# Kernel tuning notes

Hardware: AMD Instinct MI355X
Metric: run time of the kernel (lower is better)

## Reference

```python
import jax, jax.numpy as jnp
import numpy as np

N, E, G = 100000, 400000, 4096
H, C = 4, 32            # heads, hidden_dim per head
D_OUT = H * C           # 128
NODE_D, EDGE_D = 38, 13
DEC_H, OUT_D = 64, 1
NEG_SLOPE = 0.2
LN_EPS = 1e-5


def setup_inputs() -> dict:
    key = jax.random.key(0)
    ks = jax.random.split(key, 40)
    r = lambda k, s: jax.random.normal(k, s, jnp.float32) * 0.1
    inp = {
        "x": jax.random.normal(ks[0], (N, NODE_D), jnp.float32),
        "edge_index": jax.random.randint(ks[1], (2, E), 0, N),
        "edge_attr": jax.random.uniform(ks[2], (E, EDGE_D), jnp.float32),
        "batch": jnp.sort(jax.random.randint(ks[3], (N,), 0, G)),
        # --- block 1 (in=38) ---
        "Wl1": r(ks[4], (NODE_D, D_OUT)), "bl1": jnp.zeros((D_OUT,), jnp.float32),
        "Wr1": r(ks[5], (NODE_D, D_OUT)), "br1": jnp.zeros((D_OUT,), jnp.float32),
        "We1": r(ks[6], (EDGE_D, D_OUT)),
        "att1": r(ks[7], (H, C)), "ab1": jnp.zeros((D_OUT,), jnp.float32),
        "ln_g1": jnp.ones((D_OUT,), jnp.float32), "ln_b1": jnp.zeros((D_OUT,), jnp.float32),
        "Wres": r(ks[8], (NODE_D, D_OUT)), "bres": jnp.zeros((D_OUT,), jnp.float32),
        # --- block 2 (in=128, residual = identity) ---
        "Wl2": r(ks[9], (D_OUT, D_OUT)), "bl2": jnp.zeros((D_OUT,), jnp.float32),
        "Wr2": r(ks[10], (D_OUT, D_OUT)), "br2": jnp.zeros((D_OUT,), jnp.float32),
        "We2": r(ks[11], (EDGE_D, D_OUT)),
        "att2": r(ks[12], (H, C)), "ab2": jnp.zeros((D_OUT,), jnp.float32),
        "ln_g2": jnp.ones((D_OUT,), jnp.float32), "ln_b2": jnp.zeros((D_OUT,), jnp.float32),
        # --- readout MLP ---
        "Wd1": r(ks[13], (D_OUT, DEC_H)), "bd1": jnp.zeros((DEC_H,), jnp.float32),
        "Wd2": r(ks[14], (DEC_H, OUT_D)), "bd2": jnp.zeros((OUT_D,), jnp.float32),
    }
    return inp


def _segment_softmax(logits, seg, n):
    m = jax.ops.segment_max(logits, seg, num_segments=n)
    ex = jnp.exp(logits - m[seg])
    s = jax.ops.segment_sum(ex, seg, num_segments=n)
    return ex / s[seg]


def _gatv2(x, src, dst, e_feat, Wl, bl, Wr, br, We, att, ab):
    n = x.shape[0]
    xl = (x @ Wl + bl).reshape(n, H, C)   # source transform
    xr = (x @ Wr + br).reshape(n, H, C)   # target transform
    ee = (e_feat @ We).reshape(-1, H, C)  # edge transform
    z = jax.nn.leaky_relu(xl[src] + xr[dst] + ee, NEG_SLOPE)  # [E,H,C]
    logits = jnp.einsum('ehc,hc->eh', z, att)                 # [E,H]
    alpha = _segment_softmax(logits, dst, n)                  # softmax over target nbhd
    out = jax.ops.segment_sum(xl[src] * alpha[..., None], dst, num_segments=n)
    return out.reshape(n, D_OUT) + ab


def _layernorm(h, g, b):
    mu = jnp.mean(h, -1, keepdims=True)
    d = h - mu
    v = jnp.mean(d * d, -1, keepdims=True)
    return d * jax.lax.rsqrt(v + LN_EPS) * g + b


def reference(x, edge_index, edge_attr, batch,
              Wl1, bl1, Wr1, br1, We1, att1, ab1, ln_g1, ln_b1, Wres, bres,
              Wl2, bl2, Wr2, br2, We2, att2, ab2, ln_g2, ln_b2,
              Wd1, bd1, Wd2, bd2):
    src, dst = edge_index[0], edge_index[1]
    n = x.shape[0]
    # add_self_loops(fill_value='mean'): self-loop edge attr = mean of incoming edge attrs
    deg = jax.ops.segment_sum(jnp.ones((src.shape[0],), x.dtype), dst, num_segments=n)
    loop_attr = jax.ops.segment_sum(edge_attr, dst, num_segments=n) / jnp.clip(deg, 1.0)[:, None]
    nodes = jnp.arange(n)
    src_a = jnp.concatenate([src, nodes])
    dst_a = jnp.concatenate([dst, nodes])
    ea = jnp.concatenate([edge_attr, loop_attr], axis=0)

    # block 1
    h = _gatv2(x, src_a, dst_a, ea, Wl1, bl1, Wr1, br1, We1, att1, ab1)
    h = jax.nn.elu(h)
    h = _layernorm(h + (x @ Wres + bres), ln_g1, ln_b1)
    # block 2 (identity residual)
    h2 = _gatv2(h, src_a, dst_a, ea, Wl2, bl2, Wr2, br2, We2, att2, ab2)
    h2 = jax.nn.elu(h2)
    h2 = _layernorm(h2 + h, ln_g2, ln_b2)

    # global mean pool over graphs
    cnt = jax.ops.segment_sum(jnp.ones((n,), x.dtype), batch, num_segments=G)
    g = jax.ops.segment_sum(h2, batch, num_segments=G) / jnp.clip(cnt, 1.0)[:, None]

    return jax.nn.relu(g @ Wd1 + bd1) @ Wd2 + bd2
```

## Files before the change

kernel.cpp:

```cpp
#include <hip/hip_runtime.h>

typedef unsigned short u16;
typedef unsigned int   u32;
typedef __attribute__((ext_vector_type(8))) short short8;
typedef __attribute__((ext_vector_type(4))) float float4v;
typedef __attribute__((ext_vector_type(2))) float float2v;

#define NODE_D   38
#define EDGE_D   13
#define D_OUT    128
#define NEG_SLOPE 0.2f
#define LN_EPS   1e-5f

__device__ __forceinline__ float bf2f(u16 v) { return __uint_as_float(((u32)v) << 16); }
__device__ __forceinline__ u16 f2bf(float f) {
    u32 u = __float_as_uint(f);
    u += 0x7fffu + ((u >> 16) & 1u);
    return (u16)(u >> 16);
}

template <int CTRL>
__device__ __forceinline__ float dpp_radd(float x) {
    int t = __builtin_amdgcn_update_dpp(0, __float_as_int(x), CTRL, 0xf, 0xf, true);
    return x + __int_as_float(t);
}
__device__ __forceinline__ float reduce16(float p) {
    p = dpp_radd<0xB1>(p);
    p = dpp_radd<0x4E>(p);
    p = dpp_radd<0x124>(p);
    p = dpp_radd<0x128>(p);
    return p;
}
__device__ __forceinline__ float reduce64(float v) {
    v = reduce16(v);
    v += __shfl_xor(v, 16, 64);
    v += __shfl_xor(v, 32, 64);
    return v;
}

__global__ void k_pre(const int* __restrict__ dst, int E, int* __restrict__ deg,
                      const int* __restrict__ batch, int N, int G, int* __restrict__ goff,
                      const float* __restrict__ x, u16* __restrict__ xb) {
    int i = blockIdx.x * blockDim.x + threadIdx.x;
    if (i < E) atomicAdd(deg + dst[i], 1);
    if (i < N) {
        int b = batch[i];
        int prev = (i == 0) ? -1 : batch[i - 1];
        for (int g = prev + 1; g <= b; g++) goff[g] = i;
        if (i == N - 1)
            for (int g = b + 1; g <= G; g++) goff[g] = N;
    }
    if (i < N * 32) {
        int n = i >> 5, kk = (i & 31) * 2;
        float f0 = (kk < NODE_D) ? x[(size_t)n * NODE_D + kk] : 0.f;
        float f1 = (kk + 1 < NODE_D) ? x[(size_t)n * NODE_D + kk + 1] : 0.f;
        ((u32*)xb)[(size_t)n * 32 + (i & 31)] = (u32)f2bf(f0) | ((u32)f2bf(f1) << 16);
    }
}

#define SCAN_CHUNK 1024
__global__ void k_scan1(const int* __restrict__ cnt, int N, int addone, int* __restrict__ bsum) {
    __shared__ int sh[256];
    int base = blockIdx.x * SCAN_CHUNK;
    int t = threadIdx.x;
    int s = 0;
#pragma unroll
    for (int i = 0; i < 4; i++) { int idx = base + t * 4 + i; if (idx < N) s += cnt[idx] + addone; }
    sh[t] = s; __syncthreads();
    for (int ofs = 128; ofs > 0; ofs >>= 1) {
        if (t < ofs) sh[t] += sh[t + ofs];
        __syncthreads();
    }
    if (t == 0) bsum[blockIdx.x] = sh[0];
}
__global__ void k_scan2(const int* __restrict__ bsum, int nb, int* __restrict__ boff) {
    __shared__ int sh[256];
    int t = threadIdx.x;
    if (nb <= 256) {
        int v = (t < nb) ? bsum[t] : 0;
        sh[t] = v; __syncthreads();
        for (int ofs = 1; ofs < 256; ofs <<= 1) {
            int x = (t >= ofs) ? sh[t - ofs] : 0;
            __syncthreads();
            sh[t] += x;
            __syncthreads();
        }
        if (t < nb) boff[t] = sh[t] - v;
        if (t == nb - 1) boff[nb] = sh[t];
    } else if (t == 0) {
        int run = 0;
        for (int i = 0; i < nb; i++) { boff[i] = run; run += bsum[i]; }
        boff[nb] = run;
    }
}
__global__ void k_scan3(const int* __restrict__ cnt, int N, int addone,
                        const int* __restrict__ boff, int nb, int* __restrict__ off) {
    __shared__ int wtot[4];
    int base = blockIdx.x * SCAN_CHUNK;
    int t = threadIdx.x;
    int lane = t & 63, w = t >> 6;
    int v[4]; int s = 0;
#pragma unroll
    for (int i = 0; i < 4; i++) { int idx = base + t * 4 + i; v[i] = (idx < N) ? cnt[idx] + addone : 0; s += v[i]; }
    int inc = s;
#pragma unroll
    for (int ofs = 1; ofs < 64; ofs <<= 1) {
        int x = __shfl_up(inc, ofs, 64);
        if (lane >= ofs) inc += x;
    }
    if (lane == 63) wtot[w] = inc;
    __syncthreads();
    int wofs = 0;
    for (int i = 0; i < w; i++) wofs += wtot[i];
    int run = boff[blockIdx.x] + wofs + (inc - s);
#pragma unroll
    for (int i = 0; i < 4; i++) {
        int idx = base + t * 4 + i;
        if (idx < N) off[idx] = run;
        run += v[i];
    }
    if (blockIdx.x == 0 && t == 0) off[N] = boff[nb];
}

__global__ void k_fill(const int* __restrict__ src, const int* __restrict__ dst,
                       const float* __restrict__ eattr, int E,
                       const int* __restrict__ csr_off, int* __restrict__ fill,
                       int* __restrict__ csr_src, u16* __restrict__ A) {
    int e = blockIdx.x * blockDim.x + threadIdx.x;
    if (e >= E) return;
    int d = dst[e];
    int pos = csr_off[d] + atomicAdd(fill + d, 1);
    csr_src[pos] = src[e];
    u16 row[16];
#pragma unroll
    for (int k = 0; k < EDGE_D; k++) row[k] = f2bf(eattr[(size_t)e * EDGE_D + k]);
#pragma unroll
    for (int k = EDGE_D; k < 16; k++) row[k] = 0;
    uint4* rp = (uint4*)(A + (size_t)pos * 16);
    rp[0] = (uint4){(u32)row[0] | ((u32)row[1] << 16), (u32)row[2] | ((u32)row[3] << 16),
                    (u32)row[4] | ((u32)row[5] << 16), (u32)row[6] | ((u32)row[7] << 16)};
    rp[1] = (uint4){(u32)row[8] | ((u32)row[9] << 16), (u32)row[10] | ((u32)row[11] << 16),
                    (u32)row[12] | ((u32)row[13] << 16), (u32)row[14] | ((u32)row[15] << 16)};
}

__global__ void k_self(const int* __restrict__ csr_off, int N,
                       int* __restrict__ csr_src, u16* __restrict__ A) {
    int tid = blockIdx.x * blockDim.x + threadIdx.x;
    if (tid >= N * 16) return;
    int n = tid >> 4, k = tid & 15;
    int b = csr_off[n], e2 = csr_off[n + 1] - 1;
    u16 v = 0;
    if (k < EDGE_D) {
        float s = 0.f;
        for (int j = b; j < e2; j++) s += bf2f(A[(size_t)j * 16 + k]);
        v = f2bf(s / fmaxf((float)(e2 - b), 1.f));
    }
    A[(size_t)e2 * 16 + k] = v;
    if (k == 0) csr_src[e2] = n;
}

template <int KPAD, int CT, int KREAL, bool IN_BF16>
__global__ __launch_bounds__(256) void k_tf_mfma(
    const void* __restrict__ in_v,
    const float* __restrict__ W0, const float* __restrict__ b0,
    const float* __restrict__ W1, const float* __restrict__ b1,
    const float* __restrict__ W2, const float* __restrict__ b2,
    u16* __restrict__ o0, u16* __restrict__ o1, u16* __restrict__ o2,
    int N) {
    constexpr int RS = KPAD + 8;
    __shared__ u16 Bsw[CT * 16 * RS];
    __shared__ float bsh[CT * 16];
    const float* Ws[3] = {W0, W1, W2};
    const float* bs[3] = {b0, b1, b2};
    u16* outs[3] = {o0, o1, o2};
    int t = threadIdx.x;
    for (int i = t; i < CT * 16 * KPAD; i += 256) {
        int c = i / KPAD, k = i - c * KPAD;
        float v = (k < KREAL) ? Ws[c >> 7][(size_t)k * 128 + (c & 127)] : 0.f;
        Bsw[c * RS + k] = f2bf(v);
    }
    for (int i = t; i < CT * 16; i += 256) bsh[i] = bs[i >> 7][i & 127];
    __syncthreads();

    int wid = t >> 6, lane = t & 63;
    int quad = lane >> 4, m = lane & 15;

    for (int g0 = blockIdx.x * 64; g0 < N; g0 += gridDim.x * 64) {
        int na = g0 + wid * 16 + m;
        if (na > N - 1) na = N - 1;
        short8 a[KPAD / 32];
        if (IN_BF16) {
            const u16* in = (const u16*)in_v;
#pragma unroll
            for (int kc = 0; kc < KPAD / 32; kc++)
                a[kc] = *(const short8*)(in + (size_t)na * KPAD + kc * 32 + quad * 8);
        } else {
            const float* in = (const float*)in_v;
#pragma unroll
            for (int kc = 0; kc < KPAD / 32; kc++)
#pragma unroll
                for (int j = 0; j < 8; j++) {
                    int k = kc * 32 + quad * 8 + j;
                    float v = (k < KREAL) ? in[(size_t)na * KREAL + k] : 0.f;
                    a[kc][j] = (short)f2bf(v);
                }
        }
        float4v acc[CT];
#pragma unroll
        for (int ct = 0; ct < CT; ct++) acc[ct] = (float4v){0.f, 0.f, 0.f, 0.f};
#pragma unroll
        for (int ct = 0; ct < CT; ct++) {
#pragma unroll
            for (int kc = 0; kc < KPAD / 32; kc++) {
                short8 b = *(const short8*)(&Bsw[(ct * 16 + m) * RS + kc * 32 + quad * 8]);
                acc[ct] = __builtin_amdgcn_mfma_f32_16x16x32_bf16(b, a[kc], acc[ct], 0, 0, 0);
            }
        }
        int node = g0 + wid * 16 + m;
        if (node < N) {
#pragma unroll
            for (int ct = 0; ct < CT; ct++) {
                int colb = ct * 16 + quad * 4;
                u16* op = outs[colb >> 7];
                int cc = colb & 127;
                float4v bq = *(const float4v*)&bsh[colb];
                ushort4 wv;
                wv.x = f2bf(acc[ct][0] + bq[0]);
                wv.y = f2bf(acc[ct][1] + bq[1]);
                wv.z = f2bf(acc[ct][2] + bq[2]);
                wv.w = f2bf(acc[ct][3] + bq[3]);
                *(ushort4*)(op + (size_t)node * 128 + cc) = wv;
            }
        }
    }
}

__global__ __launch_bounds__(256) void k_gat(
    const int* __restrict__ csr_off, const int* __restrict__ csr_src,
    const u16* __restrict__ A_csr,
    const u16* __restrict__ xl, const u16* __restrict__ xr,
    const u16* __restrict__ res, const float* __restrict__ We,
    const float* __restrict__ att, const float* __restrict__ ab,
    const float* __restrict__ lng, const float* __restrict__ lnb,
    u16* __restrict__ hout, const int* __restrict__ batch, float* __restrict__ gsum,
    int N, int npw) {
    int t = threadIdx.x;
    int wid = t >> 6, lane = t & 63;
    int wave = blockIdx.x * 4 + wid;
    int n0 = wave * npw;
    if (n0 >= N) return;
    int n1 = n0 + npw; if (n1 > N) n1 = N;

    float2v we2[EDGE_D];
#pragma unroll
    for (int k = 0; k < EDGE_D; k++)
        we2[k] = (float2v){We[k * D_OUT + 2 * lane], We[k * D_OUT + 2 * lane + 1]};
    float a0 = att[2 * lane], a1 = att[2 * lane + 1];
    float abv0 = ab[2 * lane], abv1 = ab[2 * lane + 1];
    float lg0 = lng[2 * lane], lg1 = lng[2 * lane + 1];
    float lb0 = lnb[2 * lane], lb1 = lnb[2 * lane + 1];

    const u32* xl32 = (const u32*)xl;
    const u32* xr32 = (const u32*)xr;
    int wbeg = csr_off[n0];
    int wend = csr_off[n1];
    int nedge = wend - wbeg;

    float ps0 = 0.f, ps1 = 0.f;
    int gcur = gsum ? batch[n0] : -1;

    auto finish = [&](int n, float ssum, float2v acc2) {
        float inv = 1.f / ssum;
        float o0 = acc2[0] * inv + abv0;
        float o1 = acc2[1] * inv + abv1;
        o0 = (o0 > 0.f) ? o0 : (__expf(o0) - 1.f);
        o1 = (o1 > 0.f) ? o1 : (__expf(o1) - 1.f);
        u32 rw = ((const u32*)res)[(size_t)n * 64 + lane];
        o0 += bf2f((u16)(rw & 0xffff));
        o1 += bf2f((u16)(rw >> 16));
        float sm = reduce64(o0 + o1);
        float mu = sm * (1.f / 128.f);
        float d0 = o0 - mu, d1 = o1 - mu;
        float vv = reduce64(d0 * d0 + d1 * d1);
        float rs = rsqrtf(vv * (1.f / 128.f) + LN_EPS);
        float h0 = d0 * rs * lg0 + lb0;
        float h1 = d1 * rs * lg1 + lb1;
        if (gsum) {
            int g = batch[n];
            if (g != gcur) {
                atomicAdd(gsum + (size_t)gcur * 128 + 2 * lane, ps0);
                atomicAdd(gsum + (size_t)gcur * 128 + 2 * lane + 1, ps1);
                ps0 = 0.f; ps1 = 0.f; gcur = g;
            }
            ps0 += h0; ps1 += h1;
        } else {
            ((u32*)hout)[(size_t)n * 64 + lane] = (u32)f2bf(h0) | ((u32)f2bf(h1) << 16);
        }
    };

    const float2v z0v = (float2v){0.f, 0.f};

    if (nedge <= 64) {
        int last = nedge - 1;
        int sv = csr_src[wbeg + ((lane < nedge) ? lane : last)];
        int f0 = __builtin_amdgcn_readlane(sv, 0);
        int f1 = __builtin_amdgcn_readlane(sv, (1 <= last) ? 1 : last);
        int f2 = __builtin_amdgcn_readlane(sv, (2 <= last) ? 2 : last);
        int f3 = __builtin_amdgcn_readlane(sv, (3 <= last) ? 3 : last);
        u32 xw0 = xl32[(size_t)f0 * 64 + lane];
        u32 xw1 = xl32[(size_t)f1 * 64 + lane];
        u32 xw2 = xl32[(size_t)f2 * 64 + lane];
        u32 xw3 = xl32[(size_t)f3 * 64 + lane];
        const uint4* ap = (const uint4*)(A_csr + (size_t)wbeg * 16);
        uint4 aq0 = ap[0], aq1 = ap[1];

        int i = wbeg;
        for (int n = n0; n < n1; n++) {
            int end = csr_off[n + 1];
            u32 xrw = xr32[(size_t)n * 64 + lane];
            float2v xr2 = (float2v){bf2f((u16)(xrw & 0xffff)), bf2f((u16)(xrw >> 16))};
            float ssum = 0.f;
            float2v acc2 = (float2v){0.f, 0.f};
            for (; i < end; i++) {
                int j4 = i + 4 - wbeg; if (j4 > last) j4 = last;
                int f4 = __builtin_amdgcn_readlane(sv, j4);
                u32 xwN = xl32[(size_t)f4 * 64 + lane];
                int j1n = i + 1 - wbeg; if (j1n > last) j1n = last;
                const uint4* apn = (const uint4*)(A_csr + (size_t)(wbeg + j1n) * 16);
                uint4 an0 = apn[0], an1 = apn[1];

                u32 dw[8] = {aq0.x, aq0.y, aq0.z, aq0.w, aq1.x, aq1.y, aq1.z, aq1.w};
                float2v eeA = (float2v){0.f, 0.f}, eeB = (float2v){0.f, 0.f};
#pragma unroll
                for (int k = 0; k < EDGE_D; k++) {
                    u32 d = dw[k >> 1];
                    float av = __uint_as_float((k & 1) ? (d & 0xffff0000u) : (d << 16));
                    if ((k >> 1) & 1) eeB += we2[k] * av;
                    else             eeA += we2[k] * av;
                }
                float2v xs = (float2v){bf2f((u16)(xw0 & 0xffff)), bf2f((u16)(xw0 >> 16))};
                float2v z = (xs + xr2) + (eeA + eeB);
                float2v lz = __builtin_elementwise_max(z, z0v) + __builtin_elementwise_min(z, z0v) * NEG_SLOPE;
                float p = lz[0] * a0 + lz[1] * a1;
                p = reduce16(p);
                float wgt = __expf(p);
                ssum += wgt;
                acc2 += xs * wgt;
                xw0 = xw1; xw1 = xw2; xw2 = xw3; xw3 = xwN;
                aq0 = an0; aq1 = an1;
            }
            finish(n, ssum, acc2);
        }
    } else {
        int cl = wend - 1;
        int f = csr_src[wbeg];
        u32 xw = xl32[(size_t)f * 64 + lane];
        const uint4* ap = (const uint4*)(A_csr + (size_t)wbeg * 16);
        uint4 aq0 = ap[0], aq1 = ap[1];
        int i = wbeg;
        for (int n = n0; n < n1; n++) {
            int end = csr_off[n + 1];
            u32 xrw = xr32[(size_t)n * 64 + lane];
            float2v xr2 = (float2v){bf2f((u16)(xrw & 0xffff)), bf2f((u16)(xrw >> 16))};
            float ssum = 0.f;
            float2v acc2 = (float2v){0.f, 0.f};
            for (; i < end; i++) {
                u32 xwc = xw; uint4 q0 = aq0, q1 = aq1;
                int ip = (i + 1 < wend) ? i + 1 : cl;
                f = csr_src[ip];
                xw = xl32[(size_t)f * 64 + lane];
                const uint4* ap2 = (const uint4*)(A_csr + (size_t)ip * 16);
                aq0 = ap2[0]; aq1 = ap2[1];
                u32 dw[8] = {q0.x, q0.y, q0.z, q0.w, q1.x, q1.y, q1.z, q1.w};
                float2v eeA = (float2v){0.f, 0.f}, eeB = (float2v){0.f, 0.f};
#pragma unroll
                for (int k = 0; k < EDGE_D; k++) {
                    u32 d = dw[k >> 1];
                    float av = __uint_as_float((k & 1) ? (d & 0xffff0000u) : (d << 16));
                    if ((k >> 1) & 1) eeB += we2[k] * av;
                    else             eeA += we2[k] * av;
                }
                float2v xs = (float2v){bf2f((u16)(xwc & 0xffff)), bf2f((u16)(xwc >> 16))};
                float2v z = (xs + xr2) + (eeA + eeB);
                float2v lz = __builtin_elementwise_max(z, z0v) + __builtin_elementwise_min(z, z0v) * NEG_SLOPE;
                float p = lz[0] * a0 + lz[1] * a1;
                p = reduce16(p);
                float wgt = __expf(p);
                ssum += wgt;
                acc2 += xs * wgt;
            }
            finish(n, ssum, acc2);
        }
    }

    if (gsum) {
        atomicAdd(gsum + (size_t)gcur * 128 + 2 * lane, ps0);
        atomicAdd(gsum + (size_t)gcur * 128 + 2 * lane + 1, ps1);
    }
}

__global__ __launch_bounds__(128) void k_read(
    const float* __restrict__ gsum, const int* __restrict__ goff,
    const float* __restrict__ Wd1, const float* __restrict__ bd1,
    const float* __restrict__ Wd2, const float* __restrict__ bd2,
    float* __restrict__ out, int G) {
    __shared__ float psh[128];
    __shared__ float rsh[2][64];
    int g = blockIdx.x;
    int t = threadIdx.x;
    int cnt = goff[g + 1] - goff[g];
    float inv = 1.f / fmaxf((float)cnt, 1.f);
    psh[t] = gsum[(size_t)g * 128 + t] * inv;
    __syncthreads();
    int j = t & 63, hw = t >> 6;
    float acc = (hw == 0) ? bd1[j] : 0.f;
    int k0 = hw * 64;
    for (int k = k0; k < k0 + 64; k++)
        acc += psh[k] * Wd1[k * 64 + j];
    rsh[hw][j] = acc;
    __syncthreads();
    if (t < 64) {
        float a = fmaxf(rsh[0][t] + rsh[1][t], 0.f);
        float v = a * Wd2[t];
#pragma unroll
        for (int mk = 1; mk < 64; mk <<= 1) v += __shfl_xor(v, mk, 64);
        if (t == 0) out[g] = v + bd2[0];
    }
}

extern "C" void kernel_launch(void* const* d_in, const int* in_sizes, int n_in,
                              void* d_out, int out_size, void* d_ws, size_t ws_size,
                              hipStream_t stream) {
    const float* x     = (const float*)d_in[0];
    const int*   eidx  = (const int*)d_in[1];
    const float* eattr = (const float*)d_in[2];
    const int*   batch = (const int*)d_in[3];
    const float* Wl1 = (const float*)d_in[4],  *bl1 = (const float*)d_in[5];
    const float* Wr1 = (const float*)d_in[6],  *br1 = (const float*)d_in[7];
    const float* We1 = (const float*)d_in[8],  *att1 = (const float*)d_in[9],  *ab1 = (const float*)d_in[10];
    const float* lng1 = (const float*)d_in[11], *lnb1 = (const float*)d_in[12];
    const float* Wres = (const float*)d_in[13], *bres = (const float*)d_in[14];
    const float* Wl2 = (const float*)d_in[15], *bl2 = (const float*)d_in[16];
    const float* Wr2 = (const float*)d_in[17], *br2 = (const float*)d_in[18];
    const float* We2 = (const float*)d_in[19], *att2 = (const float*)d_in[20], *ab2 = (const float*)d_in[21];
    const float* lng2 = (const float*)d_in[22], *lnb2 = (const float*)d_in[23];
    const float* Wd1 = (const float*)d_in[24], *bd1 = (const float*)d_in[25];
    const float* Wd2 = (const float*)d_in[26], *bd2 = (const float*)d_in[27];

    int N = in_sizes[0] / NODE_D;
    int E = in_sizes[1] / 2;
    int G = out_size;
    int EN = E + N;
    const int* src = eidx;
    const int* dst = eidx + E;

    char* w = (char*)d_ws;
    auto alloc = [&](size_t bytes) -> char* {
        char* p = w;
        w += (bytes + 255) & ~(size_t)255;
        return p;
    };
    int NB = (N + SCAN_CHUNK - 1) / SCAN_CHUNK;
    int*   csr_off  = (int*)alloc((size_t)(N + 1) * 4);
    int*   csr_src  = (int*)alloc((size_t)EN * 4);
    u16*   A_csr    = (u16*)alloc((size_t)(EN + 64) * 16 * 2);
    u16*   xb       = (u16*)alloc((size_t)N * 64 * 2);
    u16*   xlb      = (u16*)alloc((size_t)N * D_OUT * 2);
    u16*   xrb      = (u16*)alloc((size_t)N * D_OUT * 2);
    u16*   resb     = (u16*)alloc((size_t)N * D_OUT * 2);
    u16*   hb       = (u16*)alloc((size_t)N * D_OUT * 2);
    int*   goff     = (int*)alloc((size_t)(G + 1) * 4);
    size_t szN = ((size_t)N * 4 + 255) & ~(size_t)255;
    size_t szG = ((size_t)G * 128 * 4 + 255) & ~(size_t)255;
    char*  zp   = alloc(2 * szN + szG);
    int*   deg  = (int*)zp;
    int*   fill = (int*)(zp + szN);
    float* gsum = (float*)(zp + 2 * szN);
    int*   bsum = (int*)alloc((size_t)(NB + 1) * 4);
    int*   boff = (int*)alloc((size_t)(NB + 1) * 4);

    hipMemsetAsync(zp, 0, 2 * szN + szG, stream);

    int mx = (E > N * 32) ? E : N * 32;
    k_pre<<<(mx + 255) / 256, 256, 0, stream>>>(dst, E, deg, batch, N, G, goff, x, xb);

    k_scan1<<<NB, 256, 0, stream>>>(deg, N, 1, bsum);
    k_scan2<<<1, 256, 0, stream>>>(bsum, NB, boff);
    k_scan3<<<NB, 256, 0, stream>>>(deg, N, 1, boff, NB, csr_off);
    k_fill<<<(E + 255) / 256, 256, 0, stream>>>(src, dst, eattr, E, csr_off, fill, csr_src, A_csr);
    k_self<<<((size_t)N * 16 + 255) / 256, 256, 0, stream>>>(csr_off, N, csr_src, A_csr);

    int npw = 4;
    int gblocks = (N + npw * 4 - 1) / (npw * 4);

    k_tf_mfma<64, 24, NODE_D, true><<<512, 256, 0, stream>>>(
        xb, Wl1, bl1, Wr1, br1, Wres, bres, xlb, xrb, resb, N);
    k_gat<<<gblocks, 256, 0, stream>>>(csr_off, csr_src, A_csr,
                                       xlb, xrb, resb, We1, att1, ab1, lng1, lnb1,
                                       hb, nullptr, nullptr, N, npw);

    k_tf_mfma<128, 16, 128, true><<<512, 256, 0, stream>>>(
        hb, Wl2, bl2, Wr2, br2, Wr2, br2, xlb, xrb, xrb, N);
    k_gat<<<gblocks, 256, 0, stream>>>(csr_off, csr_src, A_csr,
                                       xlb, xrb, hb, We2, att2, ab2, lng2, lnb2,
                                       (u16*)nullptr, batch, gsum, N, npw);

    k_read<<<G, 128, 0, stream>>>(gsum, goff, Wd1, bd1, Wd2, bd2, (float*)d_out, G);
}
```

Baseline: 544.2 us.

## Wave-parallel self-loop mean, scalar edge-attr loads, templated pooling flag

Several unrelated tweaks land together. The self-loop attribute kernel now uses one wave per node, with four row groups reducing over incoming edges through shuffles. The old version had one thread per attribute column loop serially over every edge. The GAT kernel gets a compile-time POOL template flag in place of runtime null checks, and wraps the edge-attribute row index in readfirstlane so the row address is treated as wave-uniform and can go through scalar loads. The x-to-bf16 packing also reads a float2 vector in place of two scalar loads, which assumes 8-byte alignment that NODE_D=38 keeps.

Result: no change. 540.0 us (-0.8%).

```diff
diff --git a/kernel.cpp b/kernel.cpp
--- a/kernel.cpp
+++ b/kernel.cpp
@@ -52,8 +52,11 @@
     }
     if (i < N * 32) {
         int n = i >> 5, kk = (i & 31) * 2;
-        float f0 = (kk < NODE_D) ? x[(size_t)n * NODE_D + kk] : 0.f;
-        float f1 = (kk + 1 < NODE_D) ? x[(size_t)n * NODE_D + kk + 1] : 0.f;
+        float f0 = 0.f, f1 = 0.f;
+        if (kk < NODE_D) {
+            float2v v = *(const float2v*)(x + (size_t)n * NODE_D + kk);
+            f0 = v[0]; f1 = v[1];
+        }
         ((u32*)xb)[(size_t)n * 32 + (i & 31)] = (u32)f2bf(f0) | ((u32)f2bf(f1) << 16);
     }
 }
@@ -143,20 +146,23 @@
                     (u32)row[12] | ((u32)row[13] << 16), (u32)row[14] | ((u32)row[15] << 16)};
 }
 
-__global__ void k_self(const int* __restrict__ csr_off, int N,
-                       int* __restrict__ csr_src, u16* __restrict__ A) {
-    int tid = blockIdx.x * blockDim.x + threadIdx.x;
-    if (tid >= N * 16) return;
-    int n = tid >> 4, k = tid & 15;
-    int b = csr_off[n], e2 = csr_off[n + 1] - 1;
-    u16 v = 0;
-    if (k < EDGE_D) {
-        float s = 0.f;
-        for (int j = b; j < e2; j++) s += bf2f(A[(size_t)j * 16 + k]);
-        v = f2bf(s / fmaxf((float)(e2 - b), 1.f));
-    }
-    A[(size_t)e2 * 16 + k] = v;
-    if (k == 0) csr_src[e2] = n;
+__global__ __launch_bounds__(256) void k_self(const int* __restrict__ csr_off, int N,
+                                              int* __restrict__ csr_src, u16* __restrict__ A) {
+    int wave = blockIdx.x * 4 + (threadIdx.x >> 6);
+    if (wave >= N) return;
+    int lane = threadIdx.x & 63;
+    int r = lane >> 4, k = lane & 15;
+    int b = csr_off[wave], e2 = csr_off[wave + 1] - 1;
+    float s = 0.f;
+    for (int j = b + r; j < e2; j += 4)
+        s += bf2f(A[(size_t)j * 16 + k]);
+    s += __shfl_xor(s, 16, 64);
+    s += __shfl_xor(s, 32, 64);
+    if (lane < 16) {
+        u16 v = (k < EDGE_D) ? f2bf(s / fmaxf((float)(e2 - b), 1.f)) : (u16)0;
+        A[(size_t)e2 * 16 + k] = v;
+        if (k == 0) csr_src[e2] = wave;
+    }
 }
 
 template <int KPAD, int CT, int KREAL, bool IN_BF16>
@@ -235,6 +241,7 @@
     }
 }
 
+template <bool POOL>
 __global__ __launch_bounds__(256) void k_gat(
     const int* __restrict__ csr_off, const int* __restrict__ csr_src,
     const u16* __restrict__ A_csr,
@@ -267,7 +274,7 @@
     int nedge = wend - wbeg;
 
     float ps0 = 0.f, ps1 = 0.f;
-    int gcur = gsum ? batch[n0] : -1;
+    int gcur = POOL ? batch[n0] : -1;
 
     auto finish = [&](int n, float ssum, float2v acc2) {
         float inv = 1.f / ssum;
@@ -285,7 +292,7 @@
         float rs = rsqrtf(vv * (1.f / 128.f) + LN_EPS);
         float h0 = d0 * rs * lg0 + lb0;
         float h1 = d1 * rs * lg1 + lb1;
-        if (gsum) {
+        if (POOL) {
             int g = batch[n];
             if (g != gcur) {
                 atomicAdd(gsum + (size_t)gcur * 128 + 2 * lane, ps0);
@@ -311,7 +318,8 @@
         u32 xw1 = xl32[(size_t)f1 * 64 + lane];
         u32 xw2 = xl32[(size_t)f2 * 64 + lane];
         u32 xw3 = xl32[(size_t)f3 * 64 + lane];
-        const uint4* ap = (const uint4*)(A_csr + (size_t)wbeg * 16);
+        int wbu = __builtin_amdgcn_readfirstlane(wbeg);
+        const uint4* ap = (const uint4*)(A_csr + (size_t)wbu * 16);
         uint4 aq0 = ap[0], aq1 = ap[1];
 
         int i = wbeg;
@@ -326,7 +334,8 @@
                 int f4 = __builtin_amdgcn_readlane(sv, j4);
                 u32 xwN = xl32[(size_t)f4 * 64 + lane];
                 int j1n = i + 1 - wbeg; if (j1n > last) j1n = last;
-                const uint4* apn = (const uint4*)(A_csr + (size_t)(wbeg + j1n) * 16);
+                int ipu = __builtin_amdgcn_readfirstlane(wbeg + j1n);
+                const uint4* apn = (const uint4*)(A_csr + (size_t)ipu * 16);
                 uint4 an0 = apn[0], an1 = apn[1];
 
                 u32 dw[8] = {aq0.x, aq0.y, aq0.z, aq0.w, aq1.x, aq1.y, aq1.z, aq1.w};
@@ -355,7 +364,8 @@
         int cl = wend - 1;
         int f = csr_src[wbeg];
         u32 xw = xl32[(size_t)f * 64 + lane];
-        const uint4* ap = (const uint4*)(A_csr + (size_t)wbeg * 16);
+        int wbu = __builtin_amdgcn_readfirstlane(wbeg);
+        const uint4* ap = (const uint4*)(A_csr + (size_t)wbu * 16);
         uint4 aq0 = ap[0], aq1 = ap[1];
         int i = wbeg;
         for (int n = n0; n < n1; n++) {
@@ -369,7 +379,8 @@
                 int ip = (i + 1 < wend) ? i + 1 : cl;
                 f = csr_src[ip];
                 xw = xl32[(size_t)f * 64 + lane];
-                const uint4* ap2 = (const uint4*)(A_csr + (size_t)ip * 16);
+                int ipu = __builtin_amdgcn_readfirstlane(ip);
+                const uint4* ap2 = (const uint4*)(A_csr + (size_t)ipu * 16);
                 aq0 = ap2[0]; aq1 = ap2[1];
                 u32 dw[8] = {q0.x, q0.y, q0.z, q0.w, q1.x, q1.y, q1.z, q1.w};
                 float2v eeA = (float2v){0.f, 0.f}, eeB = (float2v){0.f, 0.f};
@@ -393,7 +404,7 @@
         }
     }
 
-    if (gsum) {
+    if (POOL) {
         atomicAdd(gsum + (size_t)gcur * 128 + 2 * lane, ps0);
         atomicAdd(gsum + (size_t)gcur * 128 + 2 * lane + 1, ps1);
     }
@@ -488,22 +499,22 @@
     k_scan2<<<1, 256, 0, stream>>>(bsum, NB, boff);
     k_scan3<<<NB, 256, 0, stream>>>(deg, N, 1, boff, NB, csr_off);
     k_fill<<<(E + 255) / 256, 256, 0, stream>>>(src, dst, eattr, E, csr_off, fill, csr_src, A_csr);
-    k_self<<<((size_t)N * 16 + 255) / 256, 256, 0, stream>>>(csr_off, N, csr_src, A_csr);
+    k_self<<<(N + 3) / 4, 256, 0, stream>>>(csr_off, N, csr_src, A_csr);
 
     int npw = 4;
     int gblocks = (N + npw * 4 - 1) / (npw * 4);
 
     k_tf_mfma<64, 24, NODE_D, true><<<512, 256, 0, stream>>>(
         xb, Wl1, bl1, Wr1, br1, Wres, bres, xlb, xrb, resb, N);
-    k_gat<<<gblocks, 256, 0, stream>>>(csr_off, csr_src, A_csr,
-                                       xlb, xrb, resb, We1, att1, ab1, lng1, lnb1,
-                                       hb, nullptr, nullptr, N, npw);
+    k_gat<false><<<gblocks, 256, 0, stream>>>(csr_off, csr_src, A_csr,
+                                              xlb, xrb, resb, We1, att1, ab1, lng1, lnb1,
+                                              hb, nullptr, nullptr, N, npw);
 
     k_tf_mfma<128, 16, 128, true><<<512, 256, 0, stream>>>(
         hb, Wl2, bl2, Wr2, br2, Wr2, br2, xlb, xrb, xrb, N);
-    k_gat<<<gblocks, 256, 0, stream>>>(csr_off, csr_src, A_csr,
-                                       xlb, xrb, hb, We2, att2, ab2, lng2, lnb2,
-                                       (u16*)nullptr, batch, gsum, N, npw);
+    k_gat<true><<<gblocks, 256, 0, stream>>>(csr_off, csr_src, A_csr,
+                                             xlb, xrb, hb, We2, att2, ab2, lng2, lnb2,
+                                             (u16*)nullptr, batch, gsum, N, npw);
 
     k_read<<<G, 128, 0, stream>>>(gsum, goff, Wd1, bd1, Wd2, bd2, (float*)d_out, G);
 }
```
